# Optimization experiments

Measured on AMD Instinct MI355X. Metric: run time of the kernel, lower is better.

The kernel has to match this reference:

```python
import jax, jax.numpy as jnp
import numpy as np

N_USER = 200000
N_ITEM = 100000
N_NODES = N_USER + N_ITEM
EMB = 80            # embed_size; divisible by 5
FEAT = EMB // 5     # 16, per-feature embedding dim
N_LAYER = 3
NNZ = 1_000_000
BATCH = 4096
EMB_RATIO = 0.5
NEG_SLOPE = 0.2
EPS = 1e-12         # F.normalize clamp_min eps


def setup_inputs() -> dict:
    key = jax.random.key(0)
    ks = jax.random.split(key, 24)
    inp = {}
    inp["u_id"] = jax.random.randint(ks[0], (BATCH,), 0, N_USER)
    inp["age"] = jax.random.randint(ks[1], (BATCH,), 0, 10)
    inp["sex"] = jax.random.randint(ks[2], (BATCH,), 0, 2)
    inp["month"] = jax.random.randint(ks[3], (BATCH,), 0, 12)
    inp["day"] = jax.random.randint(ks[4], (BATCH,), 0, 31)
    inp["dow"] = jax.random.randint(ks[5], (BATCH,), 0, 7)
    inp["pos_item"] = jax.random.randint(ks[6], (BATCH,), 0, N_ITEM)
    inp["neg_item"] = jax.random.randint(ks[7], (BATCH,), 0, N_ITEM)
    # COO sparse Laplacian (one entry of lap_list)
    inp["lap_rows"] = jax.random.randint(ks[8], (NNZ,), 0, N_NODES)
    inp["lap_cols"] = jax.random.randint(ks[9], (NNZ,), 0, N_NODES)
    inp["lap_vals"] = jax.random.uniform(ks[10], (NNZ,), jnp.float32) * 0.01
    # learned parameters (kaiming-uniform-ish scale)
    inp["user_tab"] = jax.random.normal(ks[11], (N_USER, EMB), jnp.float32) * 0.1
    inp["item_tab"] = jax.random.normal(ks[12], (N_ITEM, EMB), jnp.float32) * 0.1
    inp["age_tab"] = jax.random.normal(ks[13], (10, FEAT), jnp.float32) * 0.1
    inp["sex_tab"] = jax.random.normal(ks[14], (2, FEAT), jnp.float32) * 0.1
    inp["month_tab"] = jax.random.normal(ks[15], (12, FEAT), jnp.float32) * 0.1
    inp["day_tab"] = jax.random.normal(ks[16], (31, FEAT), jnp.float32) * 0.1
    inp["dow_tab"] = jax.random.normal(ks[17], (7, FEAT), jnp.float32) * 0.1
    s = 1.0 / np.sqrt(EMB)
    inp["W1"] = jax.random.uniform(ks[18], (N_LAYER, EMB, EMB), jnp.float32, -s, s)
    inp["b1"] = jax.random.uniform(ks[19], (N_LAYER, EMB), jnp.float32, -s, s)
    inp["W2"] = jax.random.uniform(ks[20], (N_LAYER, EMB, EMB), jnp.float32, -s, s)
    inp["b2"] = jax.random.uniform(ks[21], (N_LAYER, EMB), jnp.float32, -s, s)
    return inp


def reference(u_id, age, sex, month, day, dow, pos_item, neg_item,
              lap_rows, lap_cols, lap_vals,
              user_tab, item_tab, age_tab, sex_tab, month_tab, day_tab, dow_tab,
              W1, b1, W2, b2):
    # demographic/date feature vector, concat order matches torch forward
    feats = jnp.concatenate(
        [age_tab[age], sex_tab[sex], month_tab[month], day_tab[day], dow_tab[dow]],
        axis=1)  # [B, EMB]
    # in-place .data blend of user rows (feats are detached in torch)
    blend = user_tab[u_id] * (1.0 - EMB_RATIO) + jax.lax.stop_gradient(feats) * EMB_RATIO
    updated = user_tab.at[u_id].set(blend)
    # torch mutates .data: values change, autograd sees identity -> same trick here
    user_eff = user_tab + jax.lax.stop_gradient(updated - user_tab)

    E = jnp.concatenate([user_eff, item_tab], axis=0)  # [N, EMB]
    all_E = [E]
    for i in range(N_LAYER):  # eval mode: node/message dropout off (node_flag=False)
        # sparse Laplacian matmul: L_E[r] = sum_nnz vals * E[cols]
        L_E = jax.ops.segment_sum(lap_vals[:, None] * E[lap_cols], lap_rows,
                                  num_segments=N_NODES)
        # L_E@W1+b1 + E@W1+b1 + (L_E*E)@W2+b2  (bias b1 intentionally twice, as in source)
        msg = (L_E + E) @ W1[i] + 2.0 * b1[i] + (L_E * E) @ W2[i] + b2[i]
        E = jax.nn.leaky_relu(msg, NEG_SLOPE)
        norm = E / jnp.maximum(jnp.linalg.norm(E, axis=1, keepdims=True), EPS)
        all_E.append(norm)
    all_E = jnp.concatenate(all_E, axis=1)  # [N, EMB*(L+1)]

    users = all_E[:N_USER]
    items = all_E[N_USER:]
    return users[u_id], items[pos_item], items[neg_item]
```

## Files before the change

kernel.cpp:

```cpp
#include <hip/hip_runtime.h>
#include <hip/hip_bf16.h>

#define N_USER 200000
#define N_ITEM 100000
#define N_NODES 300000
#define EMB 80
#define FEAT 16
#define NL 3
#define NNZ 1000000
#define BATCH 4096
#define OUTW 320

typedef __bf16 bf16x8 __attribute__((ext_vector_type(8)));
typedef float f32x4 __attribute__((ext_vector_type(4)));

__device__ __forceinline__ unsigned short f2bf(float f){
  union { float f; unsigned int i; } x; x.f = f;
  unsigned int i = x.i;
  unsigned int r = i + 0x7fff + ((i >> 16) & 1u);
  return (unsigned short)(r >> 16);
}
__device__ __forceinline__ float bf2f_lo(unsigned int u){
  union { unsigned int i; float f; } x; x.i = u << 16; return x.f;
}
__device__ __forceinline__ float bf2f_hi(unsigned int u){
  union { unsigned int i; float f; } x; x.i = u & 0xffff0000u; return x.f;
}

__device__ __forceinline__ void acc8(f32x4* a, uint4 u, float v){
  a[0].x += v*bf2f_lo(u.x); a[0].y += v*bf2f_hi(u.x);
  a[0].z += v*bf2f_lo(u.y); a[0].w += v*bf2f_hi(u.y);
  a[1].x += v*bf2f_lo(u.z); a[1].y += v*bf2f_hi(u.z);
  a[1].z += v*bf2f_lo(u.w); a[1].w += v*bf2f_hi(u.w);
}

__device__ __forceinline__ void combine_store(unsigned short* lp_add, unsigned short* lp_mul,
                                              const f32x4* a, uint4 u){
  float e0=bf2f_lo(u.x), e1=bf2f_hi(u.x), e2=bf2f_lo(u.y), e3=bf2f_hi(u.y);
  float e4=bf2f_lo(u.z), e5=bf2f_hi(u.z), e6=bf2f_lo(u.w), e7=bf2f_hi(u.w);
  bf16x8 av, mv;
  av[0]=(__bf16)(a[0].x+e0); av[1]=(__bf16)(a[0].y+e1);
  av[2]=(__bf16)(a[0].z+e2); av[3]=(__bf16)(a[0].w+e3);
  av[4]=(__bf16)(a[1].x+e4); av[5]=(__bf16)(a[1].y+e5);
  av[6]=(__bf16)(a[1].z+e6); av[7]=(__bf16)(a[1].w+e7);
  mv[0]=(__bf16)(a[0].x*e0); mv[1]=(__bf16)(a[0].y*e1);
  mv[2]=(__bf16)(a[0].z*e2); mv[3]=(__bf16)(a[0].w*e3);
  mv[4]=(__bf16)(a[1].x*e4); mv[5]=(__bf16)(a[1].y*e5);
  mv[6]=(__bf16)(a[1].z*e6); mv[7]=(__bf16)(a[1].w*e7);
  *(bf16x8*)lp_add = av;
  *(bf16x8*)lp_mul = mv;
}

__global__ void k_fill(float* out, int n, float v){
  int i = blockIdx.x * blockDim.x + threadIdx.x;
  if (i < n) out[i] = v;
}

__global__ void k_init(int* __restrict__ winner, int* __restrict__ rowptr){
  int i = blockIdx.x * blockDim.x + threadIdx.x;
  if (i <= N_NODES) rowptr[i] = 0;
  if (i < N_USER)   winner[i] = -1;
}

#define HIST_BLOCKS ((BATCH + NNZ + 255)/256)
#define COPY_BLOCKS ((N_NODES*EMB/4 + 255)/256)
__global__ void k_phaseB(const int* __restrict__ u_id, int* __restrict__ winner,
                         const int* __restrict__ rows, int* __restrict__ cnt,
                         const float4* __restrict__ user_tab4, const float4* __restrict__ item_tab4,
                         uint2* __restrict__ EB){
  if (blockIdx.x < HIST_BLOCKS){
    int i = blockIdx.x * 256 + threadIdx.x;
    if (i < BATCH) atomicMax(&winner[u_id[i]], i);
    int e = i - BATCH;
    if (e >= 0 && e < NNZ) atomicAdd(&cnt[rows[e]], 1);
  } else {
    int idx = (blockIdx.x - HIST_BLOCKS) * 256 + threadIdx.x;
    if (idx < N_NODES*EMB/4){
      float4 v = (idx < N_USER*EMB/4) ? user_tab4[idx] : item_tab4[idx - N_USER*EMB/4];
      uint2 o;
      o.x = (unsigned int)f2bf(v.x) | ((unsigned int)f2bf(v.y) << 16);
      o.y = (unsigned int)f2bf(v.z) | ((unsigned int)f2bf(v.w) << 16);
      EB[idx] = o;
    }
  }
}

#define SCAN_BLK 1024
#define NSCAN_BLOCKS ((N_NODES + SCAN_BLK - 1)/SCAN_BLK)
#define BF_BLOCKS ((BATCH*20 + 255)/256)
#define WT_BLOCKS ((NL*EMB*160 + NL*EMB + 255)/256)
__global__ void k_phaseC(int* __restrict__ cnt, int* __restrict__ bsum,
                         const int* __restrict__ u_id, const int* __restrict__ winner,
                         const int* __restrict__ age, const int* __restrict__ sex,
                         const int* __restrict__ month, const int* __restrict__ day,
                         const int* __restrict__ dow,
                         const float* __restrict__ user_tab,
                         const float* __restrict__ age_tab, const float* __restrict__ sex_tab,
                         const float* __restrict__ month_tab, const float* __restrict__ day_tab,
                         const float* __restrict__ dow_tab,
                         uint2* __restrict__ EB,
                         const float* __restrict__ W1, const float* __restrict__ W2,
                         const float* __restrict__ b1, const float* __restrict__ b2,
                         unsigned short* __restrict__ Wt, float* __restrict__ biasf){
  if (blockIdx.x < NSCAN_BLOCKS){
    __shared__ int s[256];
    int tid = threadIdx.x;
    int base = blockIdx.x * SCAN_BLK + tid*4;
    int v[4]; int sum = 0;
    #pragma unroll
    for (int j = 0; j < 4; j++){
      int i = base + j;
      v[j] = (i < N_NODES) ? cnt[i] : 0;
      sum += v[j];
    }
    s[tid] = sum; __syncthreads();
    int own = sum;
    for (int d = 1; d < 256; d <<= 1){
      int t = (tid >= d) ? s[tid-d] : 0;
      __syncthreads();
      s[tid] += t;
      __syncthreads();
    }
    int excl = s[tid] - own;
    if (tid == 0) bsum[blockIdx.x] = s[255];
    int run = excl;
    #pragma unroll
    for (int j = 0; j < 4; j++){
      int i = base + j;
      if (i < N_NODES) cnt[i] = run;
      run += v[j];
    }
  } else if (blockIdx.x < NSCAN_BLOCKS + BF_BLOCKS){
    int idx = (blockIdx.x - NSCAN_BLOCKS) * 256 + threadIdx.x;
    if (idx < BATCH*20){
      int b = idx / 20;
      int q = idx - b*20;
      int u = u_id[b];
      if (winner[u] == b){
        int c = q*4;
        int t = c >> 4, cc = c & 15;
        int key; const float* tab;
        switch (t){
          case 0: key = age[b];   tab = age_tab;   break;
          case 1: key = sex[b];   tab = sex_tab;   break;
          case 2: key = month[b]; tab = month_tab; break;
          case 3: key = day[b];   tab = day_tab;   break;
          default: key = dow[b];  tab = dow_tab;   break;
        }
        const float* tp = tab + key*FEAT + cc;
        const float* up = user_tab + (size_t)u*EMB + c;
        float x0 = 0.5f*up[0] + 0.5f*tp[0];
        float x1 = 0.5f*up[1] + 0.5f*tp[1];
        float x2 = 0.5f*up[2] + 0.5f*tp[2];
        float x3 = 0.5f*up[3] + 0.5f*tp[3];
        uint2 o;
        o.x = (unsigned int)f2bf(x0) | ((unsigned int)f2bf(x1) << 16);
        o.y = (unsigned int)f2bf(x2) | ((unsigned int)f2bf(x3) << 16);
        EB[(size_t)u*20 + q] = o;
      }
    }
  } else {
    int p = (blockIdx.x - NSCAN_BLOCKS - BF_BLOCKS) * 256 + threadIdx.x;
    if (p < NL*EMB*160){
      int i = p / (EMB*160);
      int rem = p - i*(EMB*160);
      int n = rem / 160;
      int k = rem - n*160;
      float v = (k < EMB) ? W1[i*EMB*EMB + k*EMB + n] : W2[i*EMB*EMB + (k-EMB)*EMB + n];
      Wt[p] = f2bf(v);
    } else if (p < NL*EMB*160 + NL*EMB){
      int t = p - NL*EMB*160;
      biasf[t] = 2.0f * b1[t] + b2[t];
    }
  }
}

__global__ void k_scan2(int* __restrict__ bsum){
  __shared__ int s[512];
  int tid = threadIdx.x;
  int v = (tid < NSCAN_BLOCKS) ? bsum[tid] : 0;
  s[tid] = v; __syncthreads();
  for (int d = 1; d < 512; d <<= 1){
    int t = (tid >= d) ? s[tid-d] : 0;
    __syncthreads();
    s[tid] += t;
    __syncthreads();
  }
  if (tid < NSCAN_BLOCKS) bsum[tid] = s[tid] - v;
}

__global__ void k_scan3(int* __restrict__ rowptr, const int* __restrict__ bsum,
                        int* __restrict__ cursor){
  int i = blockIdx.x * blockDim.x + threadIdx.x;
  if (i >= N_NODES) return;
  int v = rowptr[i] + bsum[i >> 10];
  rowptr[i] = v;
  cursor[i] = v;
  if (i == 0) rowptr[N_NODES] = NNZ;
}

__device__ __forceinline__ void gather_one(const unsigned short* __restrict__ EB,
                                           const int* __restrict__ u_id,
                                           const int* __restrict__ pos, const int* __restrict__ neg,
                                           float* __restrict__ out, int layer, int do_norm,
                                           int gw, int lane){
  int chunk = gw / BATCH;
  int b = gw - chunk*BATCH;
  int node = (chunk == 0) ? u_id[b] : ((chunk == 1) ? N_USER + pos[b] : N_USER + neg[b]);
  const unsigned short* er = EB + (size_t)node*EMB;
  union { unsigned int i; float f; } c0, c1;
  c0.i = (unsigned int)er[lane] << 16;
  float v0 = c0.f;
  float v1 = 0.f;
  if (lane < EMB-64){ c1.i = (unsigned int)er[64 + lane] << 16; v1 = c1.f; }
  float scale = 1.f;
  if (do_norm){
    float ss = v0*v0 + v1*v1;
    #pragma unroll
    for (int s = 32; s > 0; s >>= 1) ss += __shfl_xor(ss, s, 64);
    float nrm = fmaxf(sqrtf(ss), 1e-12f);
    scale = 1.f / nrm;
  }
  float* po = out + (size_t)chunk*BATCH*OUTW + (size_t)b*OUTW + layer*EMB;
  po[lane] = v0 * scale;
  if (lane < EMB-64) po[64 + lane] = v1 * scale;
}

#define SC_BLOCKS ((NNZ + 255)/256)
#define G0_BLOCKS ((3*BATCH)/4)
__global__ void k_scatter_gather0(const int* __restrict__ rows, const int* __restrict__ cols,
                                  const float* __restrict__ vals, int* __restrict__ cursor,
                                  int2* __restrict__ edges,
                                  const unsigned short* __restrict__ EB,
                                  const int* __restrict__ u_id, const int* __restrict__ pos,
                                  const int* __restrict__ neg, float* __restrict__ out){
  if (blockIdx.x < SC_BLOCKS){
    int e = blockIdx.x * 256 + threadIdx.x;
    if (e >= NNZ) return;
    int r = rows[e];
    int p = atomicAdd(&cursor[r], 1);
    int2 ed; ed.x = cols[e]; ed.y = __float_as_int(vals[e]);
    edges[p] = ed;
  } else {
    int gb = blockIdx.x - SC_BLOCKS;
    int gw = gb*4 + (threadIdx.x >> 6);
    gather_one(EB, u_id, pos, neg, out, 0, 0, gw, threadIdx.x & 63);
  }
}

#define LE_STRIDE 168
#define FB_BLOCKS ((N_NODES + 63)/64)
__launch_bounds__(256)
__global__ void k_fused2(const unsigned short* __restrict__ EBin, unsigned short* __restrict__ EBout,
                         const int* __restrict__ rowptr, const int2* __restrict__ edges,
                         const unsigned short* __restrict__ Wt, const float* __restrict__ biasf,
                         const int* __restrict__ u_id, const int* __restrict__ pos,
                         const int* __restrict__ neg, float* __restrict__ out, int glayer){
  __shared__ unsigned short la[64 * LE_STRIDE];
  int tid = threadIdx.x;

  if (blockIdx.x >= FB_BLOCKS){
    int gb = blockIdx.x - FB_BLOCKS;
    int gw = gb*4 + (tid >> 6);
    gather_one(EBin, u_id, pos, neg, out, glayer, 1, gw, tid & 63);
    return;
  }

  long row0 = (long)blockIdx.x * 64;
  int lane = tid & 63;
  int wave = tid >> 6;
  int m = lane & 15;
  int quad = lane >> 4;

  {
    int lr = tid >> 2;
    int qg = tid & 3;
    long r = row0 + lr;
    int s = 0, e = 0;
    if (r < N_NODES){ s = rowptr[r]; e = rowptr[r+1]; }
    int eo = 8*qg;
    f32x4 c0[2], c1[2], c2[2];
    c0[0]=(f32x4){0,0,0,0}; c0[1]=(f32x4){0,0,0,0};
    c1[0]=(f32x4){0,0,0,0}; c1[1]=(f32x4){0,0,0,0};
    c2[0]=(f32x4){0,0,0,0}; c2[1]=(f32x4){0,0,0,0};
    int ilast = e - 1;
    for (int i = s; i < e; i += 4){
      int rem = e - i;
      int2 ed0 = edges[i];
      int2 ed1 = edges[min(i+1, ilast)];
      int2 ed2 = edges[min(i+2, ilast)];
      int2 ed3 = edges[min(i+3, ilast)];
      float v0 = __int_as_float(ed0.y);
      float v1 = (rem > 1) ? __int_as_float(ed1.y) : 0.f;
      float v2 = (rem > 2) ? __int_as_float(ed2.y) : 0.f;
      float v3 = (rem > 3) ? __int_as_float(ed3.y) : 0.f;
      const unsigned short* g0 = EBin + (size_t)ed0.x*EMB + eo;
      const unsigned short* g1 = EBin + (size_t)ed1.x*EMB + eo;
      const unsigned short* g2 = EBin + (size_t)ed2.x*EMB + eo;
      const unsigned short* g3 = EBin + (size_t)ed3.x*EMB + eo;
      {
        uint4 u0 = *(const uint4*)(g0);
        uint4 u1 = *(const uint4*)(g1);
        uint4 u2 = *(const uint4*)(g2);
        uint4 u3 = *(const uint4*)(g3);
        acc8(c0, u0, v0); acc8(c0, u1, v1); acc8(c0, u2, v2); acc8(c0, u3, v3);
      }
      {
        uint4 u0 = *(const uint4*)(g0 + 32);
        uint4 u1 = *(const uint4*)(g1 + 32);
        uint4 u2 = *(const uint4*)(g2 + 32);
        uint4 u3 = *(const uint4*)(g3 + 32);
        acc8(c1, u0, v0); acc8(c1, u1, v1); acc8(c1, u2, v2); acc8(c1, u3, v3);
      }
      if (qg < 2){
        uint4 u0 = *(const uint4*)(g0 + 64);
        uint4 u1 = *(const uint4*)(g1 + 64);
        uint4 u2 = *(const uint4*)(g2 + 64);
        uint4 u3 = *(const uint4*)(g3 + 64);
        acc8(c2, u0, v0); acc8(c2, u1, v1); acc8(c2, u2, v2); acc8(c2, u3, v3);
      }
    }
    const unsigned short* myrow = EBin + (size_t)(r < N_NODES ? r : 0) * EMB;
    unsigned short* lp = la + lr*LE_STRIDE;
    {
      uint4 u = *(const uint4*)(myrow + eo);
      combine_store(lp + eo, lp + 80 + eo, c0, u);
    }
    {
      uint4 u = *(const uint4*)(myrow + 32 + eo);
      combine_store(lp + 32 + eo, lp + 80 + 32 + eo, c1, u);
    }
    if (qg < 2){
      uint4 u = *(const uint4*)(myrow + 64 + eo);
      combine_store(lp + 64 + eo, lp + 80 + 64 + eo, c2, u);
    }
  }

  bf16x8 bfrag[5][5];
  #pragma unroll
  for (int nt = 0; nt < 5; nt++)
    #pragma unroll
    for (int kt = 0; kt < 5; kt++)
      bfrag[nt][kt] = *(const bf16x8*)(Wt + (nt*16 + m)*160 + kt*32 + quad*8);

  asm volatile("s_waitcnt lgkmcnt(0)" ::: "memory");
  __builtin_amdgcn_sched_barrier(0);

  int arow = wave*16 + m;
  const unsigned short* lA = la + arow*LE_STRIDE;

  f32x4 acc[5];
  #pragma unroll
  for (int nt = 0; nt < 5; nt++) acc[nt] = (f32x4){0.f,0.f,0.f,0.f};

  #pragma unroll
  for (int kt = 0; kt < 5; kt++){
    bf16x8 af = *(const bf16x8*)(lA + kt*32 + quad*8);
    #pragma unroll
    for (int nt = 0; nt < 5; nt++)
      acc[nt] = __builtin_amdgcn_mfma_f32_16x16x32_bf16(af, bfrag[nt][kt], acc[nt], 0, 0, 0);
  }

  long rbase = row0 + wave*16 + quad*4;
  #pragma unroll
  for (int nt = 0; nt < 5; nt++){
    int col = nt*16 + m;
    float b = biasf[col];
    #pragma unroll
    for (int i = 0; i < 4; i++){
      long r = rbase + i;
      if (r < N_NODES){
        float v = acc[nt][i] + b;
        v = (v > 0.f) ? v : 0.2f * v;
        EBout[r*EMB + col] = f2bf(v);
      }
    }
  }
}

__global__ void k_gather_wave(const unsigned short* __restrict__ EB, const int* __restrict__ u_id,
                              const int* __restrict__ pos, const int* __restrict__ neg,
                              float* __restrict__ out, int layer, int do_norm){
  int gw = blockIdx.x * (blockDim.x >> 6) + (threadIdx.x >> 6);
  if (gw >= 3*BATCH) return;
  gather_one(EB, u_id, pos, neg, out, layer, do_norm, gw, threadIdx.x & 63);
}

extern "C" void kernel_launch(void* const* d_in, const int* in_sizes, int n_in,
                              void* d_out, int out_size, void* d_ws, size_t ws_size,
                              hipStream_t stream) {
  float* out = (float*)d_out;

  const size_t OFF_EB0    = 0;
  const size_t OFF_EB1    = 48000000;
  const size_t OFF_ROWPTR = 96000000;
  const size_t OFF_CURSOR = 97200640;
  const size_t OFF_EDGES  = 98401280;
  const size_t OFF_BSUM   = 106401280;
  const size_t OFF_WT     = 106405376;
  const size_t OFF_BIAS   = 106482176;
  const size_t OFF_WIN    = 106483200;
  const size_t NEED       = 107283200;

  float code = 0.f;
  if (ws_size < NEED)                      code = 7.f;
  else if (n_in != 22)                     code = 9.f;
  else if (in_sizes[0] != BATCH)           code = 11.f;
  else if (in_sizes[10] != NNZ)            code = 13.f;
  else if (out_size != 3*BATCH*OUTW)       code = 19.f;
  if (code != 0.f){
    k_fill<<<(out_size + 255)/256, 256, 0, stream>>>(out, out_size, code);
    return;
  }

  const int* u_id  = (const int*)d_in[0];
  const int* age   = (const int*)d_in[1];
  const int* sex   = (const int*)d_in[2];
  const int* month = (const int*)d_in[3];
  const int* day   = (const int*)d_in[4];
  const int* dow   = (const int*)d_in[5];
  const int* pos   = (const int*)d_in[6];
  const int* neg   = (const int*)d_in[7];
  const int* lrows = (const int*)d_in[8];
  const int* lcols = (const int*)d_in[9];
  const float* lvals    = (const float*)d_in[10];
  const float* user_tab = (const float*)d_in[11];
  const float* item_tab = (const float*)d_in[12];
  const float* age_tab  = (const float*)d_in[13];
  const float* sex_tab  = (const float*)d_in[14];
  const float* month_tab= (const float*)d_in[15];
  const float* day_tab  = (const float*)d_in[16];
  const float* dow_tab  = (const float*)d_in[17];
  const float* W1 = (const float*)d_in[18];
  const float* b1 = (const float*)d_in[19];
  const float* W2 = (const float*)d_in[20];
  const float* b2 = (const float*)d_in[21];

  char* ws = (char*)d_ws;
  unsigned short* EB0 = (unsigned short*)(ws + OFF_EB0);
  unsigned short* EB1 = (unsigned short*)(ws + OFF_EB1);
  int* rowptr   = (int*)(ws + OFF_ROWPTR);
  int* cursor   = (int*)(ws + OFF_CURSOR);
  int2* edges   = (int2*)(ws + OFF_EDGES);
  int* bsum     = (int*)(ws + OFF_BSUM);
  unsigned short* Wt = (unsigned short*)(ws + OFF_WT);
  float* biasf  = (float*)(ws + OFF_BIAS);
  int* winner   = (int*)(ws + OFF_WIN);

  k_init<<<(N_NODES+1+255)/256, 256, 0, stream>>>(winner, rowptr);
  k_phaseB<<<HIST_BLOCKS + COPY_BLOCKS, 256, 0, stream>>>(u_id, winner, lrows, rowptr,
      (const float4*)user_tab, (const float4*)item_tab, (uint2*)EB0);
  k_phaseC<<<NSCAN_BLOCKS + BF_BLOCKS + WT_BLOCKS, 256, 0, stream>>>(rowptr, bsum,
      u_id, winner, age, sex, month, day, dow, user_tab,
      age_tab, sex_tab, month_tab, day_tab, dow_tab,
      (uint2*)EB0, W1, W2, b1, b2, Wt, biasf);
  k_scan2<<<1, 512, 0, stream>>>(bsum);
  k_scan3<<<(N_NODES+255)/256, 256, 0, stream>>>(rowptr, bsum, cursor);
  k_scatter_gather0<<<SC_BLOCKS + G0_BLOCKS, 256, 0, stream>>>(lrows, lcols, lvals, cursor,
      edges, EB0, u_id, pos, neg, out);

  unsigned short* Ein = EB0; unsigned short* Eout = EB1;
  for (int i = 0; i < NL; i++){
    int extra = (i > 0) ? G0_BLOCKS : 0;
    k_fused2<<<FB_BLOCKS + extra, 256, 0, stream>>>(Ein, Eout, rowptr, edges,
                                                    Wt + i*EMB*160, biasf + i*EMB,
                                                    u_id, pos, neg, out, i);
    unsigned short* t = Ein; Ein = Eout; Eout = t;
  }
  k_gather_wave<<<G0_BLOCKS, 256, 0, stream>>>(Ein, u_id, pos, neg, out, NL, 1);
}
```

Baseline: 558.7 us.

## Fuse prologue kernels into one cooperative kernel with grid syncs

Replaces six separate prologue launches (init, histogram/convert, scan phases, CSR scatter, layer-0 gather) with one cooperative persistent kernel of 1024 blocks that separates phases with grid.sync(). The scan is restructured to 2048-element blocks so that a single block can scan the block sums. The goal is to remove kernel launch gaps and tail effects between the small phases. In exchange it adds grid-wide barrier cost and uses grid-stride loops over fewer threads, and it falls back to the old launches if the cooperative launch fails.

```diff
diff --git a/kernel.cpp b/kernel.cpp
--- a/kernel.cpp
+++ b/kernel.cpp
@@ -1,5 +1,8 @@
 #include <hip/hip_runtime.h>
 #include <hip/hip_bf16.h>
+#include <hip/hip_cooperative_groups.h>
+
+namespace cg = cooperative_groups;
 
 #define N_USER 200000
 #define N_ITEM 100000
@@ -54,6 +57,188 @@
 __global__ void k_fill(float* out, int n, float v){
   int i = blockIdx.x * blockDim.x + threadIdx.x;
   if (i < n) out[i] = v;
+}
+
+__device__ __forceinline__ void gather_one(const unsigned short* __restrict__ EB,
+                                           const int* __restrict__ u_id,
+                                           const int* __restrict__ pos, const int* __restrict__ neg,
+                                           float* __restrict__ out, int layer, int do_norm,
+                                           int gw, int lane){
+  int chunk = gw / BATCH;
+  int b = gw - chunk*BATCH;
+  int node = (chunk == 0) ? u_id[b] : ((chunk == 1) ? N_USER + pos[b] : N_USER + neg[b]);
+  const unsigned short* er = EB + (size_t)node*EMB;
+  union { unsigned int i; float f; } c0, c1;
+  c0.i = (unsigned int)er[lane] << 16;
+  float v0 = c0.f;
+  float v1 = 0.f;
+  if (lane < EMB-64){ c1.i = (unsigned int)er[64 + lane] << 16; v1 = c1.f; }
+  float scale = 1.f;
+  if (do_norm){
+    float ss = v0*v0 + v1*v1;
+    #pragma unroll
+    for (int s = 32; s > 0; s >>= 1) ss += __shfl_xor(ss, s, 64);
+    float nrm = fmaxf(sqrtf(ss), 1e-12f);
+    scale = 1.f / nrm;
+  }
+  float* po = out + (size_t)chunk*BATCH*OUTW + (size_t)b*OUTW + layer*EMB;
+  po[lane] = v0 * scale;
+  if (lane < EMB-64) po[64 + lane] = v1 * scale;
+}
+
+#define COOP_BLOCKS 1024
+#define COOP_THREADS 256
+#define CSCAN_BLK 2048
+#define NSC2 ((N_NODES + CSCAN_BLK - 1)/CSCAN_BLK)
+
+__global__ void k_prologue(const int* __restrict__ u_id, const int* __restrict__ age,
+                           const int* __restrict__ sex, const int* __restrict__ month,
+                           const int* __restrict__ day, const int* __restrict__ dow,
+                           const int* __restrict__ pos, const int* __restrict__ neg,
+                           const int* __restrict__ lrows, const int* __restrict__ lcols,
+                           const float* __restrict__ lvals,
+                           const float* __restrict__ user_tab, const float* __restrict__ item_tab,
+                           const float* __restrict__ age_tab, const float* __restrict__ sex_tab,
+                           const float* __restrict__ month_tab, const float* __restrict__ day_tab,
+                           const float* __restrict__ dow_tab,
+                           const float* __restrict__ W1, const float* __restrict__ b1,
+                           const float* __restrict__ W2, const float* __restrict__ b2,
+                           unsigned short* __restrict__ EB0, int* __restrict__ rowptr,
+                           int* __restrict__ cursor, int2* __restrict__ edges,
+                           int* __restrict__ bsum, unsigned short* __restrict__ Wt,
+                           float* __restrict__ biasf, int* __restrict__ winner,
+                           float* __restrict__ out){
+  cg::grid_group grid = cg::this_grid();
+  const int gtid = blockIdx.x * COOP_THREADS + threadIdx.x;
+  const int nthr = COOP_BLOCKS * COOP_THREADS;
+  __shared__ int s[256];
+
+  for (int i = gtid; i <= N_NODES; i += nthr) rowptr[i] = 0;
+  for (int i = gtid; i < N_USER; i += nthr) winner[i] = -1;
+  grid.sync();
+
+  for (int i = gtid; i < BATCH; i += nthr) atomicMax(&winner[u_id[i]], i);
+  for (int e = gtid; e < NNZ; e += nthr) atomicAdd(&rowptr[lrows[e]], 1);
+  {
+    const float4* ut4 = (const float4*)user_tab;
+    const float4* it4 = (const float4*)item_tab;
+    uint2* EB = (uint2*)EB0;
+    for (int idx = gtid; idx < N_NODES*EMB/4; idx += nthr){
+      float4 v = (idx < N_USER*EMB/4) ? ut4[idx] : it4[idx - N_USER*EMB/4];
+      uint2 o;
+      o.x = (unsigned int)f2bf(v.x) | ((unsigned int)f2bf(v.y) << 16);
+      o.y = (unsigned int)f2bf(v.z) | ((unsigned int)f2bf(v.w) << 16);
+      EB[idx] = o;
+    }
+  }
+  for (int p = gtid; p < NL*EMB*160 + NL*EMB; p += nthr){
+    if (p < NL*EMB*160){
+      int i = p / (EMB*160);
+      int rem = p - i*(EMB*160);
+      int n = rem / 160;
+      int k = rem - n*160;
+      float v = (k < EMB) ? W1[i*EMB*EMB + k*EMB + n] : W2[i*EMB*EMB + (k-EMB)*EMB + n];
+      Wt[p] = f2bf(v);
+    } else {
+      int t = p - NL*EMB*160;
+      biasf[t] = 2.0f * b1[t] + b2[t];
+    }
+  }
+  grid.sync();
+
+  if (blockIdx.x < NSC2){
+    int tid = threadIdx.x;
+    int base = blockIdx.x * CSCAN_BLK + tid*8;
+    int v[8]; int sum = 0;
+    #pragma unroll
+    for (int j = 0; j < 8; j++){
+      int i = base + j;
+      v[j] = (i < N_NODES) ? rowptr[i] : 0;
+      sum += v[j];
+    }
+    s[tid] = sum; __syncthreads();
+    int own = sum;
+    for (int d = 1; d < 256; d <<= 1){
+      int t = (tid >= d) ? s[tid-d] : 0;
+      __syncthreads();
+      s[tid] += t;
+      __syncthreads();
+    }
+    int excl = s[tid] - own;
+    if (tid == 0) bsum[blockIdx.x] = s[255];
+    int run = excl;
+    #pragma unroll
+    for (int j = 0; j < 8; j++){
+      int i = base + j;
+      if (i < N_NODES) rowptr[i] = run;
+      run += v[j];
+    }
+  } else {
+    int idx = (blockIdx.x - NSC2) * COOP_THREADS + threadIdx.x;
+    if (idx < BATCH*20){
+      int b = idx / 20;
+      int q = idx - b*20;
+      int u = u_id[b];
+      if (winner[u] == b){
+        int c = q*4;
+        int t = c >> 4, cc = c & 15;
+        int key; const float* tab;
+        switch (t){
+          case 0: key = age[b];   tab = age_tab;   break;
+          case 1: key = sex[b];   tab = sex_tab;   break;
+          case 2: key = month[b]; tab = month_tab; break;
+          case 3: key = day[b];   tab = day_tab;   break;
+          default: key = dow[b];  tab = dow_tab;   break;
+        }
+        const float* tp = tab + key*FEAT + cc;
+        const float* up = user_tab + (size_t)u*EMB + c;
+        float x0 = 0.5f*up[0] + 0.5f*tp[0];
+        float x1 = 0.5f*up[1] + 0.5f*tp[1];
+        float x2 = 0.5f*up[2] + 0.5f*tp[2];
+        float x3 = 0.5f*up[3] + 0.5f*tp[3];
+        uint2 o;
+        o.x = (unsigned int)f2bf(x0) | ((unsigned int)f2bf(x1) << 16);
+        o.y = (unsigned int)f2bf(x2) | ((unsigned int)f2bf(x3) << 16);
+        ((uint2*)EB0)[(size_t)u*20 + q] = o;
+      }
+    }
+  }
+  grid.sync();
+
+  if (blockIdx.x == 0){
+    int tid = threadIdx.x;
+    int v = (tid < NSC2) ? bsum[tid] : 0;
+    s[tid] = v; __syncthreads();
+    for (int d = 1; d < 256; d <<= 1){
+      int t = (tid >= d) ? s[tid-d] : 0;
+      __syncthreads();
+      s[tid] += t;
+      __syncthreads();
+    }
+    if (tid < NSC2) bsum[tid] = s[tid] - v;
+  }
+  grid.sync();
+
+  for (int i = gtid; i < N_NODES; i += nthr){
+    int v = rowptr[i] + bsum[i >> 11];
+    rowptr[i] = v;
+    cursor[i] = v;
+  }
+  if (gtid == 0) rowptr[N_NODES] = NNZ;
+  grid.sync();
+
+  for (int e = gtid; e < NNZ; e += nthr){
+    int r = lrows[e];
+    int p = atomicAdd(&cursor[r], 1);
+    int2 ed; ed.x = lcols[e]; ed.y = __float_as_int(lvals[e]);
+    edges[p] = ed;
+  }
+  {
+    int wglobal = blockIdx.x*4 + (threadIdx.x >> 6);
+    int lane = threadIdx.x & 63;
+    for (int gw = wglobal; gw < 3*BATCH; gw += COOP_BLOCKS*4)
+      gather_one(EB0, u_id, pos, neg, out, 0, 0, gw, lane);
+  }
 }
 
 __global__ void k_init(int* __restrict__ winner, int* __restrict__ rowptr){
@@ -197,33 +382,6 @@
   rowptr[i] = v;
   cursor[i] = v;
   if (i == 0) rowptr[N_NODES] = NNZ;
-}
-
-__device__ __forceinline__ void gather_one(const unsigned short* __restrict__ EB,
-                                           const int* __restrict__ u_id,
-                                           const int* __restrict__ pos, const int* __restrict__ neg,
-                                           float* __restrict__ out, int layer, int do_norm,
-                                           int gw, int lane){
-  int chunk = gw / BATCH;
-  int b = gw - chunk*BATCH;
-  int node = (chunk == 0) ? u_id[b] : ((chunk == 1) ? N_USER + pos[b] : N_USER + neg[b]);
-  const unsigned short* er = EB + (size_t)node*EMB;
-  union { unsigned int i; float f; } c0, c1;
-  c0.i = (unsigned int)er[lane] << 16;
-  float v0 = c0.f;
-  float v1 = 0.f;
-  if (lane < EMB-64){ c1.i = (unsigned int)er[64 + lane] << 16; v1 = c1.f; }
-  float scale = 1.f;
-  if (do_norm){
-    float ss = v0*v0 + v1*v1;
-    #pragma unroll
-    for (int s = 32; s > 0; s >>= 1) ss += __shfl_xor(ss, s, 64);
-    float nrm = fmaxf(sqrtf(ss), 1e-12f);
-    scale = 1.f / nrm;
-  }
-  float* po = out + (size_t)chunk*BATCH*OUTW + (size_t)b*OUTW + layer*EMB;
-  po[lane] = v0 * scale;
-  if (lane < EMB-64) po[64 + lane] = v1 * scale;
 }
 
 #define SC_BLOCKS ((NNZ + 255)/256)
@@ -447,17 +605,31 @@
   float* biasf  = (float*)(ws + OFF_BIAS);
   int* winner   = (int*)(ws + OFF_WIN);
 
-  k_init<<<(N_NODES+1+255)/256, 256, 0, stream>>>(winner, rowptr);
-  k_phaseB<<<HIST_BLOCKS + COPY_BLOCKS, 256, 0, stream>>>(u_id, winner, lrows, rowptr,
-      (const float4*)user_tab, (const float4*)item_tab, (uint2*)EB0);
-  k_phaseC<<<NSCAN_BLOCKS + BF_BLOCKS + WT_BLOCKS, 256, 0, stream>>>(rowptr, bsum,
-      u_id, winner, age, sex, month, day, dow, user_tab,
-      age_tab, sex_tab, month_tab, day_tab, dow_tab,
-      (uint2*)EB0, W1, W2, b1, b2, Wt, biasf);
-  k_scan2<<<1, 512, 0, stream>>>(bsum);
-  k_scan3<<<(N_NODES+255)/256, 256, 0, stream>>>(rowptr, bsum, cursor);
-  k_scatter_gather0<<<SC_BLOCKS + G0_BLOCKS, 256, 0, stream>>>(lrows, lcols, lvals, cursor,
-      edges, EB0, u_id, pos, neg, out);
+  void* args[] = {
+    (void*)&u_id, (void*)&age, (void*)&sex, (void*)&month, (void*)&day, (void*)&dow,
+    (void*)&pos, (void*)&neg, (void*)&lrows, (void*)&lcols, (void*)&lvals,
+    (void*)&user_tab, (void*)&item_tab, (void*)&age_tab, (void*)&sex_tab,
+    (void*)&month_tab, (void*)&day_tab, (void*)&dow_tab,
+    (void*)&W1, (void*)&b1, (void*)&W2, (void*)&b2,
+    (void*)&EB0, (void*)&rowptr, (void*)&cursor, (void*)&edges, (void*)&bsum,
+    (void*)&Wt, (void*)&biasf, (void*)&winner, (void*)&out
+  };
+  hipError_t cerr = hipLaunchCooperativeKernel((void*)k_prologue,
+      dim3(COOP_BLOCKS), dim3(COOP_THREADS), args, 0, stream);
+
+  if (cerr != hipSuccess){
+    k_init<<<(N_NODES+1+255)/256, 256, 0, stream>>>(winner, rowptr);
+    k_phaseB<<<HIST_BLOCKS + COPY_BLOCKS, 256, 0, stream>>>(u_id, winner, lrows, rowptr,
+        (const float4*)user_tab, (const float4*)item_tab, (uint2*)EB0);
+    k_phaseC<<<NSCAN_BLOCKS + BF_BLOCKS + WT_BLOCKS, 256, 0, stream>>>(rowptr, bsum,
+        u_id, winner, age, sex, month, day, dow, user_tab,
+        age_tab, sex_tab, month_tab, day_tab, dow_tab,
+        (uint2*)EB0, W1, W2, b1, b2, Wt, biasf);
+    k_scan2<<<1, 512, 0, stream>>>(bsum);
+    k_scan3<<<(N_NODES+255)/256, 256, 0, stream>>>(rowptr, bsum, cursor);
+    k_scatter_gather0<<<SC_BLOCKS + G0_BLOCKS, 256, 0, stream>>>(lrows, lcols, lvals, cursor,
+        edges, EB0, u_id, pos, neg, out);
+  }
 
   unsigned short* Ein = EB0; unsigned short* Eout = EB1;
   for (int i = 0; i < NL; i++){
```

New measurement: 1.108 ms. +98.2%, slower.
